# Kernel optimization log

Measured on AMD Instinct MI355X. Metric: run time of the kernel, lower is better.

Reference implementation:

```python
import jax, jax.numpy as jnp
import numpy as np

B, T = 32, 128
D, H, HD = 512, 8, 64
FF, E, N = 2048, 8, 3
NF = 16            # Fourier features
VOCAB, FEAT = 119, 200
SCALE = 10.0
EPS = 1e-5


def layernorm(x, g, b):
    m = jnp.mean(x, axis=-1, keepdims=True)
    v = jnp.mean((x - m) ** 2, axis=-1, keepdims=True)
    return (x - m) * jax.lax.rsqrt(v + EPS) * g + b


def setup_inputs() -> dict:
    key = jax.random.key(0)
    ks = jax.random.split(key, 32)
    f32 = jnp.float32
    inp = {
        "src": jax.random.randint(ks[0], (B, T), 0, VOCAB),
        "frac": jax.random.uniform(ks[1], (B, T), dtype=f32),
        "embed_table": jax.random.normal(ks[2], (VOCAB, FEAT), f32),
        "W_m2v": jax.random.normal(ks[3], (FEAT, D), f32) * 0.05,
        "b_m2v": jnp.zeros((D,), f32),
        "pb_W": jax.random.normal(ks[4], (1, NF), f32) * 0.1,
        "pb_b": jax.random.uniform(ks[5], (NF,), f32) * 2 * np.pi,
        "pb_a": jax.random.normal(ks[6], (NF,), f32),
        "Wk": jax.random.normal(ks[7], (N, D, D), f32) * 0.03,
        "bk": jnp.zeros((N, D), f32),
        "Wv": jax.random.normal(ks[8], (N, D, D), f32) * 0.03,
        "bv": jnp.zeros((N, D), f32),
        "Wo": jax.random.normal(ks[9], (N, D, D), f32) * 0.03,
        "bo": jnp.zeros((N, D), f32),
        "ln1_g": jnp.ones((N, D), f32),
        "ln1_b": jnp.zeros((N, D), f32),
        "ln2_g": jnp.ones((N, D), f32),
        "ln2_b": jnp.zeros((N, D), f32),
        "gate_W": jax.random.normal(ks[10], (N, D, E), f32) * 0.05,
        "gate_b": jnp.zeros((N, E), f32),
        "eW1": jax.random.normal(ks[11], (N, E, D, FF), f32) * 0.03,
        "eb1": jnp.zeros((N, E, FF), f32),
        "eW2": jax.random.normal(ks[12], (N, E, FF, D), f32) * 0.02,
        "eb2": jnp.zeros((N, E, D), f32),
    }
    return inp


def reference(src, frac, embed_table, W_m2v, b_m2v, pb_W, pb_b, pb_a,
              Wk, bk, Wv, bv, Wo, bo, ln1_g, ln1_b, ln2_g, ln2_b,
              gate_W, gate_b, eW1, eb1, eW2, eb2):
    # Embedder: mat2vec lookup + linear projection
    x = embed_table[src] @ W_m2v + b_m2v                      # [B,T,D]

    # Fourier positional bias: pb[b,i,j] = cos((frac_j - frac_i)*scale * W + b) @ a
    diffs = (frac[:, None, :] - frac[:, :, None]) * SCALE     # [B,T,T]
    rff = jnp.cos(diffs[..., None] * pb_W[0] + pb_b)          # [B,T,T,NF]
    pb = rff @ pb_a                                           # [B,T,T]

    for i in range(N):
        # --- Fourier-bias attention ---
        K = (x @ Wk[i] + bk[i]).reshape(B, T, H, HD).transpose(0, 2, 1, 3)  # [B,H,T,HD]
        V = (x @ Wv[i] + bv[i]).reshape(B, T, H, HD).transpose(0, 2, 1, 3)
        # scores[b,h,i,j,d] = K[b,h,j,d] + pb[b,i,j]; weighted = sum_j scores*V
        # factor: sum_j K*V (indep of i) + sum_j pb[b,i,j]*V[b,h,j,d]
        kv = jnp.sum(K * V, axis=2)                           # [B,H,HD]
        pbv = jnp.einsum('bij,bhjd->bhid', pb, V)             # [B,H,T,HD]
        wv = (pbv + kv[:, :, None, :]).transpose(0, 2, 1, 3).reshape(B, T, D)
        x = layernorm(x + wv @ Wo[i] + bo[i], ln1_g[i], ln1_b[i])

        # --- MoE FFN, top-2 gating (eval mode: no dropout/noise) ---
        probs = jax.nn.softmax(x @ gate_W[i] + gate_b[i], axis=-1)   # [B,T,E]
        top2_s, top2_e = jax.lax.top_k(probs, 2)                     # [B,T,2]
        w = jnp.sum(jax.nn.one_hot(top2_e, E, dtype=x.dtype) * top2_s[..., None], axis=2)  # [B,T,E]
        h = jax.nn.relu(jnp.einsum('btd,edf->btef', x, eW1[i]) + eb1[i])  # [B,T,E,FF]
        eo = jnp.einsum('btef,efd->bted', h, eW2[i]) + eb2[i]             # [B,T,E,D]
        ff = jnp.einsum('bte,bted->btd', w, eo)
        x = layernorm(x + ff, ln2_g[i], ln2_b[i])
    return x
```

## Files before the change

kernel.cpp:

```cpp
#include <hip/hip_runtime.h>
#include <math.h>

#define B_    32
#define T_    128
#define D_    512
#define FF_   2048
#define E_    8
#define NL_   3
#define NF_   16
#define FEAT_ 200
#define BT_   4096

typedef short bf16x8 __attribute__((ext_vector_type(8)));
typedef float f32x4  __attribute__((ext_vector_type(4)));

__device__ inline unsigned short f2bf(float f) {
    unsigned u = __float_as_uint(f);
    unsigned r = (u + 0x7fffu + ((u >> 16) & 1u)) >> 16;
    return (unsigned short)r;
}
__device__ inline void split_bf(float f, unsigned short& h, unsigned short& l) {
    h = f2bf(f);
    float fh = __uint_as_float(((unsigned)h) << 16);
    l = f2bf(f - fh);
}

__device__ __forceinline__ void ld_g2l(const unsigned short* g, unsigned short* l)
{
    __builtin_amdgcn_global_load_lds(
        (const __attribute__((address_space(1))) unsigned int*)(uintptr_t)g,
        (__attribute__((address_space(3))) unsigned int*)(uintptr_t)l,
        16, 0, 0);
}

template <int MODE, bool SPLITOUT, bool RELU>
__global__ __launch_bounds__(256)
void mgemm_k(const unsigned short* __restrict__ Ah, const unsigned short* __restrict__ Al,
             const unsigned short* __restrict__ Bh, const unsigned short* __restrict__ Bl,
             const float* __restrict__ bias,
             float* __restrict__ Cf, unsigned short* __restrict__ Ch,
             unsigned short* __restrict__ Cl,
             int M, int K, int N, long strB, int strBias,
             const int* __restrict__ counts, const int* __restrict__ offsets,
             const int* __restrict__ tok_list)
{
    const int z  = blockIdx.z;
    const int m0 = blockIdx.y * 128, n0 = blockIdx.x * 128;
    int rows, rowoff = 0;
    if constexpr (MODE != 0) {
        rows = counts[z];
        if (m0 >= rows) return;
        rowoff = offsets[z];
    } else {
        rows = M;
    }
    const unsigned short* Bhb = Bh + (long)z * strB;
    const unsigned short* Blb = Bl + (long)z * strB;
    const float* biasb = bias + (long)z * strBias;

    __shared__ unsigned short S0[128 * 32];
    __shared__ unsigned short S1[128 * 32];
    __shared__ unsigned short S2[128 * 32];
    __shared__ unsigned short S3[128 * 32];

    const int tid  = threadIdx.x;
    const int w    = tid >> 6, lane = tid & 63;
    const int wm = w & 1, wn = w >> 1;
    const int l15 = lane & 15, quad = lane >> 4;

    const int lrow0 = w * 32 + (lane >> 2);
    const int lrow1 = lrow0 + 16;
    const int sseg  = (lane & 3) ^ ((lane >> 3) & 3);
    const int lb0   = (w * 2 + 0) * 512;
    const int lb1   = (w * 2 + 1) * 512;

    long ga0, ga1;
    if constexpr (MODE == 1) {
        int m_a = m0 + lrow0; if (m_a >= rows) m_a = rows - 1;
        int m_b = m0 + lrow1; if (m_b >= rows) m_b = rows - 1;
        ga0 = tok_list[z * BT_ + m_a];
        ga1 = tok_list[z * BT_ + m_b];
    } else if constexpr (MODE == 2) {
        int m_a = m0 + lrow0; if (m_a >= rows) m_a = rows - 1;
        int m_b = m0 + lrow1; if (m_b >= rows) m_b = rows - 1;
        ga0 = (long)rowoff + m_a;
        ga1 = (long)rowoff + m_b;
    } else {
        ga0 = m0 + lrow0;
        ga1 = m0 + lrow1;
    }
    const long aoff0 = ga0 * (long)K + sseg * 8;
    const long aoff1 = ga1 * (long)K + sseg * 8;
    const long boff0 = (long)(n0 + lrow0) * K + sseg * 8;
    const long boff1 = (long)(n0 + lrow1) * K + sseg * 8;

    f32x4 acc[4][4];
#pragma unroll
    for (int i = 0; i < 4; ++i)
#pragma unroll
        for (int j = 0; j < 4; ++j) acc[i][j] = (f32x4)0.f;

    const int xq = quad ^ ((l15 >> 1) & 3);

    for (int k0 = 0; k0 < K; k0 += 32) {
        __syncthreads();
        ld_g2l(Ah  + aoff0 + k0, S0 + lb0);
        ld_g2l(Ah  + aoff1 + k0, S0 + lb1);
        ld_g2l(Al  + aoff0 + k0, S1 + lb0);
        ld_g2l(Al  + aoff1 + k0, S1 + lb1);
        ld_g2l(Bhb + boff0 + k0, S2 + lb0);
        ld_g2l(Bhb + boff1 + k0, S2 + lb1);
        ld_g2l(Blb + boff0 + k0, S3 + lb0);
        ld_g2l(Blb + boff1 + k0, S3 + lb1);
        __syncthreads();

        bf16x8 ah4[4], al4[4], bh4[4], bl4[4];
#pragma unroll
        for (int i = 0; i < 4; ++i) {
            int ro = (wm * 64 + i * 16 + l15) * 32 + xq * 8;
            ah4[i] = *(const bf16x8*)&S0[ro];
            al4[i] = *(const bf16x8*)&S1[ro];
        }
#pragma unroll
        for (int j = 0; j < 4; ++j) {
            int ro = (wn * 64 + j * 16 + l15) * 32 + xq * 8;
            bh4[j] = *(const bf16x8*)&S2[ro];
            bl4[j] = *(const bf16x8*)&S3[ro];
        }
#pragma unroll
        for (int i = 0; i < 4; ++i)
#pragma unroll
            for (int j = 0; j < 4; ++j) {
                acc[i][j] = __builtin_amdgcn_mfma_f32_16x16x32_bf16(al4[i], bh4[j], acc[i][j], 0, 0, 0);
                acc[i][j] = __builtin_amdgcn_mfma_f32_16x16x32_bf16(ah4[i], bl4[j], acc[i][j], 0, 0, 0);
                acc[i][j] = __builtin_amdgcn_mfma_f32_16x16x32_bf16(ah4[i], bh4[j], acc[i][j], 0, 0, 0);
            }
    }

#pragma unroll
    for (int i = 0; i < 4; ++i) {
#pragma unroll
        for (int r = 0; r < 4; ++r) {
            int gm = m0 + wm * 64 + i * 16 + quad * 4 + r;
            if (MODE != 0 && gm >= rows) continue;
            long crow = (MODE != 0) ? ((long)rowoff + gm) : (long)gm;
#pragma unroll
            for (int j = 0; j < 4; ++j) {
                int col = n0 + wn * 64 + j * 16 + l15;
                float v = acc[i][j][r] + biasb[col];
                if constexpr (RELU) v = fmaxf(v, 0.f);
                if constexpr (SPLITOUT) {
                    unsigned short h, l;
                    split_bf(v, h, l);
                    Ch[crow * (long)N + col] = h;
                    Cl[crow * (long)N + col] = l;
                } else {
                    Cf[crow * (long)N + col] = v;
                }
            }
        }
    }
}

__global__ __launch_bounds__(256)
void gemm_k(const float* __restrict__ A, const float* __restrict__ Bm,
            const float* __restrict__ bias, float* __restrict__ C,
            int K, int lda, int ldb, int ldc,
            long strA, long strB, long strC, int strBias)
{
    const int z  = blockIdx.z;
    const int m0 = blockIdx.y * 64, n0 = blockIdx.x * 64;
    const float* Ab    = A    + (long)z * strA;
    const float* Bb    = Bm   + (long)z * strB;
    const float* biasb = bias + (long)z * strBias;
    float*       Cb    = C    + (long)z * strC;

    __shared__ float As[16][68];
    __shared__ float Bs[16][64];

    const int tid = threadIdx.x;
    const int tx  = tid & 15, ty = tid >> 4;
    const int ar  = tid >> 2;
    const int akc = (tid & 3) * 4;
    const float* Arow = Ab + (long)(m0 + ar) * lda;
    const int bkr = tid >> 4;
    const int bnc = (tid & 15) * 4;

    float acc[4][4];
#pragma unroll
    for (int i = 0; i < 4; ++i)
#pragma unroll
        for (int j = 0; j < 4; ++j) acc[i][j] = 0.f;

    for (int k0 = 0; k0 < K; k0 += 16) {
        if (k0 + 16 <= K) {
            float4 a = *(const float4*)(Arow + k0 + akc);
            As[akc + 0][ar] = a.x; As[akc + 1][ar] = a.y;
            As[akc + 2][ar] = a.z; As[akc + 3][ar] = a.w;
        } else {
#pragma unroll
            for (int j = 0; j < 4; ++j) {
                int kk = k0 + akc + j;
                As[akc + j][ar] = (kk < K) ? Arow[kk] : 0.f;
            }
        }
        {
            int kk = k0 + bkr;
            float4 b;
            if (kk < K) b = *(const float4*)(Bb + (long)kk * ldb + n0 + bnc);
            else        b = make_float4(0.f, 0.f, 0.f, 0.f);
            *(float4*)&Bs[bkr][bnc] = b;
        }
        __syncthreads();
#pragma unroll
        for (int k = 0; k < 16; ++k) {
            float4 av = *(const float4*)&As[k][ty * 4];
            float4 bv = *(const float4*)&Bs[k][tx * 4];
            float am[4] = {av.x, av.y, av.z, av.w};
            float bn[4] = {bv.x, bv.y, bv.z, bv.w};
#pragma unroll
            for (int i = 0; i < 4; ++i)
#pragma unroll
                for (int j = 0; j < 4; ++j)
                    acc[i][j] = fmaf(am[i], bn[j], acc[i][j]);
        }
        __syncthreads();
    }
#pragma unroll
    for (int i = 0; i < 4; ++i) {
        float*       Cp = Cb + (long)(m0 + ty * 4 + i) * ldc + n0 + tx * 4;
        const float* bp = biasb + n0 + tx * 4;
#pragma unroll
        for (int j = 0; j < 4; ++j) Cp[j] = acc[i][j] + bp[j];
    }
}

__global__ __launch_bounds__(256)
void transpose_split_k(const float* __restrict__ in,
                       unsigned short* __restrict__ oh, unsigned short* __restrict__ ol,
                       int R, int C, long strIn, long strOut)
{
    __shared__ float tile[32][33];
    const float* I = in + (long)blockIdx.z * strIn;
    unsigned short* OH = oh + (long)blockIdx.z * strOut;
    unsigned short* OL = ol + (long)blockIdx.z * strOut;
    int c0 = blockIdx.x * 32, r0 = blockIdx.y * 32;
    int tx = threadIdx.x & 31, ty = threadIdx.x >> 5;
#pragma unroll
    for (int i = 0; i < 4; ++i)
        tile[ty + i * 8][tx] = I[(long)(r0 + ty + i * 8) * C + c0 + tx];
    __syncthreads();
#pragma unroll
    for (int i = 0; i < 4; ++i) {
        unsigned short h, l;
        split_bf(tile[tx][ty + i * 8], h, l);
        long o = (long)(c0 + ty + i * 8) * R + r0 + tx;
        OH[o] = h; OL[o] = l;
    }
}

__global__ void cvt_split_k(const float* __restrict__ in,
                            unsigned short* __restrict__ oh,
                            unsigned short* __restrict__ ol, int n)
{
    int i = blockIdx.x * 256 + threadIdx.x;
    if (i < n) {
        unsigned short h, l;
        split_bf(in[i], h, l);
        oh[i] = h; ol[i] = l;
    }
}

__global__ void bias_cat_k(const float* __restrict__ a, const float* __restrict__ b,
                           float* __restrict__ o)
{
    int i = blockIdx.x * 256 + threadIdx.x;
    o[i] = (i < D_) ? a[i] : b[i - D_];
}

__global__ void embed_gather_k(const int* __restrict__ src,
                               const float* __restrict__ table,
                               float* __restrict__ emb)
{
    int t = blockIdx.x;
    int v = src[t];
    for (int k = threadIdx.x; k < FEAT_; k += 256)
        emb[t * FEAT_ + k] = table[v * FEAT_ + k];
}

__global__ __launch_bounds__(256)
void pb_k(const float* __restrict__ frac, const float* __restrict__ pbW,
          const float* __restrict__ pbb, const float* __restrict__ pba,
          float* __restrict__ pb)
{
    int idx = blockIdx.x * 256 + threadIdx.x;
    int b = idx >> 14;
    int i = (idx >> 7) & 127;
    int j = idx & 127;
    float diff = (frac[b * T_ + j] - frac[b * T_ + i]) * 10.0f;
    float s = 0.f;
#pragma unroll
    for (int f = 0; f < NF_; ++f)
        s = fmaf(cosf(fmaf(diff, pbW[f], pbb[f])), pba[f], s);
    pb[idx] = s;
}

__global__ __launch_bounds__(256)
void kv_k(const float* __restrict__ KV, float* __restrict__ kv)
{
    int idx = blockIdx.x * 256 + threadIdx.x;
    int b = idx >> 9, c = idx & 511;
    const float* Kp = KV + (long)b * T_ * 1024 + c;
    float s = 0.f;
    for (int t = 0; t < T_; ++t) {
        const float* p = Kp + t * 1024;
        s = fmaf(p[0], p[D_], s);
    }
    kv[idx] = s;
}

__global__ __launch_bounds__(256)
void ln_res_k(const float* __restrict__ x, const float* __restrict__ add,
              const float* __restrict__ g, const float* __restrict__ b,
              float* __restrict__ out, unsigned short* __restrict__ oh,
              unsigned short* __restrict__ ol)
{
    int wave = threadIdx.x >> 6, lane = threadIdx.x & 63;
    int row = blockIdx.x * 4 + wave;
    const float* xr = x   + (long)row * D_ + lane * 8;
    const float* ar = add + (long)row * D_ + lane * 8;
    float v[8]; float s = 0.f;
#pragma unroll
    for (int j = 0; j < 8; ++j) { v[j] = xr[j] + ar[j]; s += v[j]; }
#pragma unroll
    for (int off = 32; off > 0; off >>= 1) s += __shfl_xor(s, off, 64);
    float mean = s * (1.f / D_);
    float q = 0.f;
#pragma unroll
    for (int j = 0; j < 8; ++j) { float d = v[j] - mean; q += d * d; }
#pragma unroll
    for (int off = 32; off > 0; off >>= 1) q += __shfl_xor(q, off, 64);
    float inv = rsqrtf(q * (1.f / D_) + 1e-5f);
    float* orow = out + (long)row * D_ + lane * 8;
    unsigned short* hrow = oh + (long)row * D_ + lane * 8;
    unsigned short* lrow = ol + (long)row * D_ + lane * 8;
#pragma unroll
    for (int j = 0; j < 8; ++j) {
        int c = lane * 8 + j;
        float o = (v[j] - mean) * inv * g[c] + b[c];
        orow[j] = o;
        unsigned short hh, ll;
        split_bf(o, hh, ll);
        hrow[j] = hh; lrow[j] = ll;
    }
}

__global__ __launch_bounds__(256)
void ln_moe_k(const float* __restrict__ x, const float* __restrict__ eo,
              const int* __restrict__ tok_slot, const float* __restrict__ tok_w,
              const int* __restrict__ offsets,
              const float* __restrict__ g, const float* __restrict__ b,
              float* __restrict__ out, unsigned short* __restrict__ oh,
              unsigned short* __restrict__ ol)
{
    int wave = threadIdx.x >> 6, lane = threadIdx.x & 63;
    int row = blockIdx.x * 4 + wave;
    int  c0 = tok_slot[row * 2], c1 = tok_slot[row * 2 + 1];
    float w0 = tok_w[row * 2],  w1 = tok_w[row * 2 + 1];
    long r0 = offsets[c0 >> 12] + (c0 & 4095);
    long r1 = offsets[c1 >> 12] + (c1 & 4095);
    const float* xr = x  + (long)row * D_ + lane * 8;
    const float* e0 = eo + r0 * D_ + lane * 8;
    const float* e1 = eo + r1 * D_ + lane * 8;
    float v[8]; float s = 0.f;
#pragma unroll
    for (int j = 0; j < 8; ++j) {
        v[j] = xr[j] + w0 * e0[j] + w1 * e1[j];
        s += v[j];
    }
#pragma unroll
    for (int off = 32; off > 0; off >>= 1) s += __shfl_xor(s, off, 64);
    float mean = s * (1.f / D_);
    float q = 0.f;
#pragma unroll
    for (int j = 0; j < 8; ++j) { float d = v[j] - mean; q += d * d; }
#pragma unroll
    for (int off = 32; off > 0; off >>= 1) q += __shfl_xor(q, off, 64);
    float inv = rsqrtf(q * (1.f / D_) + 1e-5f);
    float* orow = out + (long)row * D_ + lane * 8;
    unsigned short* hrow = oh + (long)row * D_ + lane * 8;
    unsigned short* lrow = ol + (long)row * D_ + lane * 8;
#pragma unroll
    for (int j = 0; j < 8; ++j) {
        int c = lane * 8 + j;
        float o = (v[j] - mean) * inv * g[c] + b[c];
        orow[j] = o;
        unsigned short hh, ll;
        split_bf(o, hh, ll);
        hrow[j] = hh; lrow[j] = ll;
    }
}

__global__ __launch_bounds__(256)
void gate_k(const float* __restrict__ x, const float* __restrict__ gW,
            const float* __restrict__ gb, int* __restrict__ counts,
            int* __restrict__ tok_list, int* __restrict__ tok_slot,
            float* __restrict__ tok_w)
{
    int wave = threadIdx.x >> 6, lane = threadIdx.x & 63;
    int t = blockIdx.x * 4 + wave;
    float acc[8];
#pragma unroll
    for (int e = 0; e < 8; ++e) acc[e] = 0.f;
    const float* xr = x + (long)t * D_;
#pragma unroll
    for (int j = 0; j < 8; ++j) {
        int d = lane * 8 + j;
        float xv = xr[d];
        const float* w = gW + d * 8;
#pragma unroll
        for (int e = 0; e < 8; ++e) acc[e] = fmaf(xv, w[e], acc[e]);
    }
#pragma unroll
    for (int off = 32; off > 0; off >>= 1)
#pragma unroll
        for (int e = 0; e < 8; ++e) acc[e] += __shfl_xor(acc[e], off, 64);

    if (lane == 0) {
        float m = -1e30f;
#pragma unroll
        for (int e = 0; e < 8; ++e) { acc[e] += gb[e]; m = fmaxf(m, acc[e]); }
        float p[8]; float s = 0.f;
#pragma unroll
        for (int e = 0; e < 8; ++e) { p[e] = expf(acc[e] - m); s += p[e]; }
        float inv = 1.f / s;
        int e1 = 0;
        for (int e = 1; e < 8; ++e) if (p[e] > p[e1]) e1 = e;
        int e2 = -1;
        for (int e = 0; e < 8; ++e) {
            if (e == e1) continue;
            if (e2 < 0 || p[e] > p[e2]) e2 = e;
        }
        int s1 = atomicAdd(&counts[e1], 1);
        tok_list[e1 * BT_ + s1] = t;
        tok_slot[t * 2]     = (e1 << 12) | s1;
        tok_w[t * 2]        = p[e1] * inv;
        int s2 = atomicAdd(&counts[e2], 1);
        tok_list[e2 * BT_ + s2] = t;
        tok_slot[t * 2 + 1] = (e2 << 12) | s2;
        tok_w[t * 2 + 1]    = p[e2] * inv;
    }
}

__global__ void zero_counts_k(int* __restrict__ counts)
{
    if (threadIdx.x < E_) counts[threadIdx.x] = 0;
}

__global__ void scan_k(const int* __restrict__ counts, int* __restrict__ offsets)
{
    if (threadIdx.x == 0) {
        int s = 0;
        for (int e = 0; e < E_; ++e) { offsets[e] = s; s += counts[e]; }
    }
}

extern "C" void kernel_launch(void* const* d_in, const int* in_sizes, int n_in,
                              void* d_out, int out_size, void* d_ws, size_t ws_size,
                              hipStream_t stream)
{
    const int*   src   = (const int*)  d_in[0];
    const float* frac  = (const float*)d_in[1];
    const float* table = (const float*)d_in[2];
    const float* W_m2v = (const float*)d_in[3];
    const float* b_m2v = (const float*)d_in[4];
    const float* pbW   = (const float*)d_in[5];
    const float* pbb   = (const float*)d_in[6];
    const float* pba   = (const float*)d_in[7];
    const float* Wk    = (const float*)d_in[8];
    const float* bk    = (const float*)d_in[9];
    const float* Wv    = (const float*)d_in[10];
    const float* bv    = (const float*)d_in[11];
    const float* Wo    = (const float*)d_in[12];
    const float* bo    = (const float*)d_in[13];
    const float* ln1g  = (const float*)d_in[14];
    const float* ln1b  = (const float*)d_in[15];
    const float* ln2g  = (const float*)d_in[16];
    const float* ln2b  = (const float*)d_in[17];
    const float* gW    = (const float*)d_in[18];
    const float* gb    = (const float*)d_in[19];
    const float* eW1   = (const float*)d_in[20];
    const float* eb1   = (const float*)d_in[21];
    const float* eW2   = (const float*)d_in[22];
    const float* eb2   = (const float*)d_in[23];

    float* ws   = (float*)d_ws;
    float* x    = ws;  ws += (long)BT_ * D_;
    float* pb   = ws;  ws += (long)B_ * T_ * T_;
    float* eo   = ws;  ws += (long)2 * BT_ * D_;
    float* kv   = ws;  ws += B_ * D_;
    float* tokw = ws;  ws += 2 * BT_;
    float* kvbias = ws; ws += 2 * D_;
    unsigned short* us = (unsigned short*)ws;
    unsigned short* x_h   = us;  us += (long)BT_ * D_;
    unsigned short* x_l   = us;  us += (long)BT_ * D_;
    unsigned short* Wkv_h = us;  us += (long)2 * D_ * D_;
    unsigned short* Wkv_l = us;  us += (long)2 * D_ * D_;
    unsigned short* Wo_h  = us;  us += (long)D_ * D_;
    unsigned short* Wo_l  = us;  us += (long)D_ * D_;
    unsigned short* e1_h  = us;  us += (long)E_ * FF_ * D_;
    unsigned short* e1_l  = us;  us += (long)E_ * FF_ * D_;
    unsigned short* e2_h  = us;  us += (long)E_ * D_ * FF_;
    unsigned short* e2_l  = us;  us += (long)E_ * D_ * FF_;
    int* counts  = (int*)us;
    int* offsets = counts + 8;
    int* toklist = offsets + 8;
    int* tokslot = toklist + E_ * BT_;
    char* ar = (char*)(tokslot + 2 * BT_);
    ar = (char*)(((size_t)ar + 255) & ~(size_t)255);
    unsigned short* h_h = (unsigned short*)ar;
    unsigned short* h_l = h_h + (long)2 * BT_ * FF_;
    float* emb  = (float*)ar;
    float* KVb  = emb + (long)BT_ * FEAT_;
    float* wv   = KVb + (long)BT_ * 2 * D_;
    float* tmp  = wv  + (long)BT_ * D_;
    unsigned short* wv_h = (unsigned short*)(tmp + (long)BT_ * D_);
    unsigned short* wv_l = wv_h + (long)BT_ * D_;

    embed_gather_k<<<BT_, 256, 0, stream>>>(src, table, emb);
    gemm_k<<<dim3(8, 64, 1), 256, 0, stream>>>(
        emb, W_m2v, b_m2v, x, FEAT_, FEAT_, D_, D_, 0, 0, 0, 0);
    cvt_split_k<<<(BT_ * D_) / 256, 256, 0, stream>>>(x, x_h, x_l, BT_ * D_);

    pb_k<<<(B_ * T_ * T_) / 256, 256, 0, stream>>>(frac, pbW, pbb, pba, pb);

    for (int i = 0; i < NL_; ++i) {
        transpose_split_k<<<dim3(16, 16, 1), 256, 0, stream>>>(
            Wk + (long)i * D_ * D_, Wkv_h, Wkv_l, D_, D_, 0, 0);
        transpose_split_k<<<dim3(16, 16, 1), 256, 0, stream>>>(
            Wv + (long)i * D_ * D_, Wkv_h + (long)D_ * D_, Wkv_l + (long)D_ * D_,
            D_, D_, 0, 0);
        transpose_split_k<<<dim3(16, 16, 1), 256, 0, stream>>>(
            Wo + (long)i * D_ * D_, Wo_h, Wo_l, D_, D_, 0, 0);
        transpose_split_k<<<dim3(64, 16, E_), 256, 0, stream>>>(
            eW1 + (long)i * E_ * D_ * FF_, e1_h, e1_l, D_, FF_,
            (long)D_ * FF_, (long)FF_ * D_);
        transpose_split_k<<<dim3(16, 64, E_), 256, 0, stream>>>(
            eW2 + (long)i * E_ * FF_ * D_, e2_h, e2_l, FF_, D_,
            (long)FF_ * D_, (long)D_ * FF_);
        bias_cat_k<<<4, 256, 0, stream>>>(bk + i * D_, bv + i * D_, kvbias);

        mgemm_k<0, false, false><<<dim3(8, 32, 1), 256, 0, stream>>>(
            x_h, x_l, Wkv_h, Wkv_l, kvbias,
            KVb, nullptr, nullptr, BT_, D_, 2 * D_, 0, 0,
            nullptr, nullptr, nullptr);

        kv_k<<<(B_ * D_) / 256, 256, 0, stream>>>(KVb, kv);

        gemm_k<<<dim3(8, 2, B_), 256, 0, stream>>>(
            pb, KVb + D_, kv, wv, T_, T_, 2 * D_, D_,
            (long)T_ * T_, (long)T_ * 2 * D_, (long)T_ * D_, D_);
        cvt_split_k<<<(BT_ * D_) / 256, 256, 0, stream>>>(wv, wv_h, wv_l, BT_ * D_);

        mgemm_k<0, false, false><<<dim3(4, 32, 1), 256, 0, stream>>>(
            wv_h, wv_l, Wo_h, Wo_l, bo + i * D_,
            tmp, nullptr, nullptr, BT_, D_, D_, 0, 0, nullptr, nullptr, nullptr);

        ln_res_k<<<BT_ / 4, 256, 0, stream>>>(x, tmp, ln1g + i * D_, ln1b + i * D_,
                                              x, x_h, x_l);

        zero_counts_k<<<1, 64, 0, stream>>>(counts);
        gate_k<<<BT_ / 4, 256, 0, stream>>>(x, gW + (long)i * D_ * E_, gb + i * E_,
                                            counts, toklist, tokslot, tokw);
        scan_k<<<1, 1, 0, stream>>>(counts, offsets);

        mgemm_k<1, true, true><<<dim3(16, 32, E_), 256, 0, stream>>>(
            x_h, x_l, e1_h, e1_l, eb1 + (long)i * E_ * FF_,
            nullptr, h_h, h_l, 0, D_, FF_,
            (long)FF_ * D_, FF_, counts, offsets, toklist);
        mgemm_k<2, false, false><<<dim3(4, 32, E_), 256, 0, stream>>>(
            h_h, h_l, e2_h, e2_l, eb2 + (long)i * E_ * D_,
            eo, nullptr, nullptr, 0, FF_, D_,
            (long)D_ * FF_, D_, counts, offsets, toklist);

        float* dst = (i == NL_ - 1) ? (float*)d_out : x;
        ln_moe_k<<<BT_ / 4, 256, 0, stream>>>(x, eo, tokslot, tokw, offsets,
                                              ln2g + i * D_, ln2b + i * D_,
                                              dst, x_h, x_l);
    }
}
```

Before: 1.478 ms.

## Double-buffer LDS tiles in split-bf16 MFMA GEMM and fuse split conversion into epilogue

```diff
diff --git a/kernel.cpp b/kernel.cpp
--- a/kernel.cpp
+++ b/kernel.cpp
@@ -58,10 +58,7 @@
     const unsigned short* Blb = Bl + (long)z * strB;
     const float* biasb = bias + (long)z * strBias;
 
-    __shared__ unsigned short S0[128 * 32];
-    __shared__ unsigned short S1[128 * 32];
-    __shared__ unsigned short S2[128 * 32];
-    __shared__ unsigned short S3[128 * 32];
+    __shared__ unsigned short S[2][4 * 4096];
 
     const int tid  = threadIdx.x;
     const int w    = tid >> 6, lane = tid & 63;
@@ -102,30 +99,48 @@
 
     const int xq = quad ^ ((l15 >> 1) & 3);
 
+    {
+        unsigned short* Sb = S[0];
+        ld_g2l(Ah  + aoff0, Sb + 0 * 4096 + lb0);
+        ld_g2l(Ah  + aoff1, Sb + 0 * 4096 + lb1);
+        ld_g2l(Al  + aoff0, Sb + 1 * 4096 + lb0);
+        ld_g2l(Al  + aoff1, Sb + 1 * 4096 + lb1);
+        ld_g2l(Bhb + boff0, Sb + 2 * 4096 + lb0);
+        ld_g2l(Bhb + boff1, Sb + 2 * 4096 + lb1);
+        ld_g2l(Blb + boff0, Sb + 3 * 4096 + lb0);
+        ld_g2l(Blb + boff1, Sb + 3 * 4096 + lb1);
+    }
+
+    unsigned short* Scur = S[0];
+    unsigned short* Snxt = S[1];
+
     for (int k0 = 0; k0 < K; k0 += 32) {
         __syncthreads();
-        ld_g2l(Ah  + aoff0 + k0, S0 + lb0);
-        ld_g2l(Ah  + aoff1 + k0, S0 + lb1);
-        ld_g2l(Al  + aoff0 + k0, S1 + lb0);
-        ld_g2l(Al  + aoff1 + k0, S1 + lb1);
-        ld_g2l(Bhb + boff0 + k0, S2 + lb0);
-        ld_g2l(Bhb + boff1 + k0, S2 + lb1);
-        ld_g2l(Blb + boff0 + k0, S3 + lb0);
-        ld_g2l(Blb + boff1 + k0, S3 + lb1);
-        __syncthreads();
+
+        if (k0 + 32 < K) {
+            int kn = k0 + 32;
+            ld_g2l(Ah  + aoff0 + kn, Snxt + 0 * 4096 + lb0);
+            ld_g2l(Ah  + aoff1 + kn, Snxt + 0 * 4096 + lb1);
+            ld_g2l(Al  + aoff0 + kn, Snxt + 1 * 4096 + lb0);
+            ld_g2l(Al  + aoff1 + kn, Snxt + 1 * 4096 + lb1);
+            ld_g2l(Bhb + boff0 + kn, Snxt + 2 * 4096 + lb0);
+            ld_g2l(Bhb + boff1 + kn, Snxt + 2 * 4096 + lb1);
+            ld_g2l(Blb + boff0 + kn, Snxt + 3 * 4096 + lb0);
+            ld_g2l(Blb + boff1 + kn, Snxt + 3 * 4096 + lb1);
+        }
 
         bf16x8 ah4[4], al4[4], bh4[4], bl4[4];
 #pragma unroll
         for (int i = 0; i < 4; ++i) {
             int ro = (wm * 64 + i * 16 + l15) * 32 + xq * 8;
-            ah4[i] = *(const bf16x8*)&S0[ro];
-            al4[i] = *(const bf16x8*)&S1[ro];
+            ah4[i] = *(const bf16x8*)&Scur[0 * 4096 + ro];
+            al4[i] = *(const bf16x8*)&Scur[1 * 4096 + ro];
         }
 #pragma unroll
         for (int j = 0; j < 4; ++j) {
             int ro = (wn * 64 + j * 16 + l15) * 32 + xq * 8;
-            bh4[j] = *(const bf16x8*)&S2[ro];
-            bl4[j] = *(const bf16x8*)&S3[ro];
+            bh4[j] = *(const bf16x8*)&Scur[2 * 4096 + ro];
+            bl4[j] = *(const bf16x8*)&Scur[3 * 4096 + ro];
         }
 #pragma unroll
         for (int i = 0; i < 4; ++i)
@@ -135,6 +150,8 @@
                 acc[i][j] = __builtin_amdgcn_mfma_f32_16x16x32_bf16(ah4[i], bl4[j], acc[i][j], 0, 0, 0);
                 acc[i][j] = __builtin_amdgcn_mfma_f32_16x16x32_bf16(ah4[i], bh4[j], acc[i][j], 0, 0, 0);
             }
+
+        unsigned short* t = Scur; Scur = Snxt; Snxt = t;
     }
 
 #pragma unroll
@@ -162,9 +179,11 @@
     }
 }
 
+template <bool WF32, bool SPLIT>
 __global__ __launch_bounds__(256)
 void gemm_k(const float* __restrict__ A, const float* __restrict__ Bm,
             const float* __restrict__ bias, float* __restrict__ C,
+            unsigned short* __restrict__ Oh, unsigned short* __restrict__ Ol,
             int K, int lda, int ldb, int ldc,
             long strA, long strB, long strC, int strBias)
 {
@@ -173,7 +192,6 @@
     const float* Ab    = A    + (long)z * strA;
     const float* Bb    = Bm   + (long)z * strB;
     const float* biasb = bias + (long)z * strBias;
-    float*       Cb    = C    + (long)z * strC;
 
     __shared__ float As[16][68];
     __shared__ float Bs[16][64];
@@ -228,10 +246,21 @@
     }
 #pragma unroll
     for (int i = 0; i < 4; ++i) {
-        float*       Cp = Cb + (long)(m0 + ty * 4 + i) * ldc + n0 + tx * 4;
+        long row = (long)z * (strC / 1) + 0;
+        (void)row;
+        long base = ((long)z * strC) + (long)(m0 + ty * 4 + i) * ldc + n0 + tx * 4;
         const float* bp = biasb + n0 + tx * 4;
 #pragma unroll
-        for (int j = 0; j < 4; ++j) Cp[j] = acc[i][j] + bp[j];
+        for (int j = 0; j < 4; ++j) {
+            float v = acc[i][j] + bp[j];
+            if constexpr (WF32) C[base + j] = v;
+            if constexpr (SPLIT) {
+                unsigned short h, l;
+                split_bf(v, h, l);
+                Oh[base + j] = h;
+                Ol[base + j] = l;
+            }
+        }
     }
 }
 
@@ -256,18 +285,6 @@
         split_bf(tile[tx][ty + i * 8], h, l);
         long o = (long)(c0 + ty + i * 8) * R + r0 + tx;
         OH[o] = h; OL[o] = l;
-    }
-}
-
-__global__ void cvt_split_k(const float* __restrict__ in,
-                            unsigned short* __restrict__ oh,
-                            unsigned short* __restrict__ ol, int n)
-{
-    int i = blockIdx.x * 256 + threadIdx.x;
-    if (i < n) {
-        unsigned short h, l;
-        split_bf(in[i], h, l);
-        oh[i] = h; ol[i] = l;
     }
 }
 
@@ -522,15 +539,13 @@
     unsigned short* h_l = h_h + (long)2 * BT_ * FF_;
     float* emb  = (float*)ar;
     float* KVb  = emb + (long)BT_ * FEAT_;
-    float* wv   = KVb + (long)BT_ * 2 * D_;
-    float* tmp  = wv  + (long)BT_ * D_;
+    float* tmp  = KVb + (long)BT_ * 2 * D_;
     unsigned short* wv_h = (unsigned short*)(tmp + (long)BT_ * D_);
     unsigned short* wv_l = wv_h + (long)BT_ * D_;
 
     embed_gather_k<<<BT_, 256, 0, stream>>>(src, table, emb);
-    gemm_k<<<dim3(8, 64, 1), 256, 0, stream>>>(
-        emb, W_m2v, b_m2v, x, FEAT_, FEAT_, D_, D_, 0, 0, 0, 0);
-    cvt_split_k<<<(BT_ * D_) / 256, 256, 0, stream>>>(x, x_h, x_l, BT_ * D_);
+    gemm_k<true, true><<<dim3(8, 64, 1), 256, 0, stream>>>(
+        emb, W_m2v, b_m2v, x, x_h, x_l, FEAT_, FEAT_, D_, D_, 0, 0, 0, 0);
 
     pb_k<<<(B_ * T_ * T_) / 256, 256, 0, stream>>>(frac, pbW, pbb, pba, pb);
 
@@ -557,10 +572,9 @@
 
         kv_k<<<(B_ * D_) / 256, 256, 0, stream>>>(KVb, kv);
 
-        gemm_k<<<dim3(8, 2, B_), 256, 0, stream>>>(
-            pb, KVb + D_, kv, wv, T_, T_, 2 * D_, D_,
+        gemm_k<false, true><<<dim3(8, 2, B_), 256, 0, stream>>>(
+            pb, KVb + D_, kv, nullptr, wv_h, wv_l, T_, T_, 2 * D_, D_,
             (long)T_ * T_, (long)T_ * 2 * D_, (long)T_ * D_, D_);
-        cvt_split_k<<<(BT_ * D_) / 256, 256, 0, stream>>>(wv, wv_h, wv_l, BT_ * D_);
 
         mgemm_k<0, false, false><<<dim3(4, 32, 1), 256, 0, stream>>>(
             wv_h, wv_l, Wo_h, Wo_l, bo + i * D_,
```

Result: faster. 1.355 ms (-8.3%).
